# Optimization experiments

Measured on AMD Instinct MI355X. Metric: run time of the kernel, lower is better.

The kernel has to match this reference:

```python
import jax, jax.numpy as jnp
import numpy as np

N = 50000   # nodes
E = 800000  # edges (avg degree 16)
D = 128     # in/hid size
C = 64      # out classes
L = 3       # layers
EPS = 1e-5


def setup_inputs() -> dict:
    key = jax.random.key(0)
    ks = jax.random.split(key, 8)
    x = jax.random.normal(ks[0], (N, D), dtype=jnp.float32)
    src = jax.random.randint(ks[1], (E,), 0, N)
    dst = jax.random.randint(ks[2], (E,), 0, N)
    s = 1.0 / np.sqrt(D)
    Wself = jax.random.normal(ks[3], (L, D, D), dtype=jnp.float32) * s
    Wneigh = jax.random.normal(ks[4], (L, D, D), dtype=jnp.float32) * s
    b_conv = jnp.zeros((L, D), dtype=jnp.float32)
    gamma = jnp.ones((L - 1, D), dtype=jnp.float32)
    beta = jnp.zeros((L - 1, D), dtype=jnp.float32)
    Wout = jax.random.normal(ks[5], (D, C), dtype=jnp.float32) * s
    bout = jnp.zeros((C,), dtype=jnp.float32)
    return {"x": x, "src": src, "dst": dst, "Wself": Wself, "Wneigh": Wneigh,
            "b_conv": b_conv, "gamma": gamma, "beta": beta, "Wout": Wout, "bout": bout}


def _layernorm(h, g, b):
    mu = jnp.mean(h, axis=-1, keepdims=True)
    var = jnp.mean(jnp.square(h - mu), axis=-1, keepdims=True)
    return g * (h - mu) * jax.lax.rsqrt(var + EPS) + b


def reference(x, src, dst, Wself, Wneigh, b_conv, gamma, beta, Wout, bout):
    # in-degree per destination node, clamped to >= 1 (DGL mean semantics)
    deg = jax.ops.segment_sum(jnp.ones((E,), dtype=x.dtype), dst, num_segments=N)
    inv_deg = 1.0 / jnp.maximum(deg, 1.0)  # [N]
    h = x
    for i in range(L):
        h_res = h
        # mean aggregation: gather src feats, scatter-add to dst, normalize
        agg = jax.ops.segment_sum(h[src], dst, num_segments=N) * inv_deg[:, None]
        # SAGEConv: fc_self(h) + fc_neigh(agg) + bias
        h = h @ Wself[i] + agg @ Wneigh[i] + b_conv[i]
        h = h + h_res  # residual (shapes always match: D == hid)
        if i != L - 1:
            h = jax.nn.relu(h)
            h = _layernorm(h, gamma[i], beta[i])
            # dropout omitted (eval mode)
    embedding = h
    logits = embedding @ Wout + bout
    return (logits, embedding)
```

## Files before the change

kernel.cpp:

```cpp
#include <hip/hip_runtime.h>

#define NN 50000
#define EE 800000
#define DD 128
#define CC 64
#define LDA 264

#define BSH 7
#define NBKT ((NN + (1 << BSH) - 1) >> BSH)
#define BCAP 3072
#define EPB 4096

typedef unsigned short u16;
typedef unsigned int u32;
typedef __attribute__((ext_vector_type(8))) short short8;
typedef __attribute__((ext_vector_type(4))) float f32x4;

__device__ __forceinline__ float bf2f(u16 u) {
    union { u32 i; float f; } v; v.i = ((u32)u) << 16; return v.f;
}
__device__ __forceinline__ u16 f2bf(float f) {
    union { float f; u32 i; } v; v.f = f;
    u32 x = v.i;
    u32 r = x + 0x7fffu + ((x >> 16) & 1u);
    return (u16)(r >> 16);
}


__global__ __launch_bounds__(1024) void k_bucket(const int* __restrict__ src,
                                                 const int* __restrict__ dst,
                                                 int* __restrict__ bcnt,
                                                 u32* __restrict__ bkt) {
    __shared__ int cnt[NBKT];
    __shared__ int base[NBKT];
    int t = threadIdx.x;
    int e0 = blockIdx.x * EPB;
    for (int i = t; i < NBKT; i += 1024) cnt[i] = 0;
    __syncthreads();
    int bk[4], lp[4];
    u32 pk[4];
#pragma unroll
    for (int j = 0; j < 4; ++j) {
        int e = e0 + t + 1024 * j;
        if (e < EE) {
            int d = dst[e];
            int s = src[e];
            bk[j] = d >> BSH;
            pk[j] = (u32)s | ((u32)(d & 127) << 16);
            lp[j] = atomicAdd(&cnt[bk[j]], 1);
        } else {
            bk[j] = -1;
        }
    }
    __syncthreads();
    for (int i = t; i < NBKT; i += 1024)
        base[i] = atomicAdd(&bcnt[i], cnt[i]);
    __syncthreads();
#pragma unroll
    for (int j = 0; j < 4; ++j) {
        if (bk[j] >= 0)
            bkt[(size_t)bk[j] * BCAP + base[bk[j]] + lp[j]] = pk[j];
    }
}


__global__ __launch_bounds__(512) void k_fill2(const int* __restrict__ bcnt,
                                               const u32* __restrict__ bkt,
                                               int* __restrict__ row_off,
                                               float* __restrict__ inv_deg,
                                               int* __restrict__ csr) {
    __shared__ int cnt[128];
    __shared__ int off[128];
    __shared__ int wtot;
    int b = blockIdx.x;
    int t = threadIdx.x;
    int lane = t & 63;
    int n = bcnt[b];

    int part = 0;
    for (int i = lane; i < b; i += 64) part += bcnt[i];
#pragma unroll
    for (int o = 1; o < 64; o <<= 1) part += __shfl_xor(part, o);
    int gbase = part;

    if (t < 128) cnt[t] = 0;
    __syncthreads();

    const u32* bp = bkt + (size_t)b * BCAP;
    int dl[6], sv[6], lp[6];
#pragma unroll
    for (int j = 0; j < 6; ++j) {
        int i = t + 512 * j;
        if (i < n) {
            u32 pk = bp[i];
            dl[j] = (int)(pk >> 16) & 127;
            sv[j] = (int)(pk & 0xffffu);
            lp[j] = atomicAdd(&cnt[dl[j]], 1);
        } else {
            dl[j] = -1;
        }
    }
    __syncthreads();

    int x = 0, v = 0;
    if (t < 128) {
        v = cnt[t];
        x = v;
#pragma unroll
        for (int o = 1; o < 64; o <<= 1) {
            int y = __shfl_up(x, o, 64);
            if (lane >= o) x += y;
        }
        if (t == 63) wtot = x;
    }
    __syncthreads();
    if (t < 128) {
        int excl = x - v + ((t >= 64) ? wtot : 0);
        off[t] = excl;
        int node = (b << BSH) + t;
        if (node < NN) {
            row_off[node] = gbase + excl;
            inv_deg[node] = 1.0f / fmaxf((float)v, 1.0f);
        } else if (node == NN) {
            row_off[NN] = gbase + excl;
        }
    }
    __syncthreads();

    int* cp = csr + gbase;
#pragma unroll
    for (int j = 0; j < 6; ++j) {
        if (dl[j] >= 0) cp[off[dl[j]] + lp[j]] = sv[j];
    }
}


__global__ __launch_bounds__(256) void k_x2bf(const float* __restrict__ x,
                                              u16* __restrict__ xb) {
    int i = (blockIdx.x * 256 + threadIdx.x) * 4;
    if (i < NN * DD) {
        float4 v = *(const float4*)(x + i);
        uint2 p;
        p.x = (u32)f2bf(v.x) | ((u32)f2bf(v.y) << 16);
        p.y = (u32)f2bf(v.z) | ((u32)f2bf(v.w) << 16);
        *(uint2*)(xb + i) = p;
    }
}


__global__ __launch_bounds__(256) void k_wpack(const float* __restrict__ Ws,
                                               const float* __restrict__ Wn,
                                               u16* __restrict__ wpk) {
    int tid = blockIdx.x * 256 + threadIdx.x;
    if (tid >= 3 * 4096) return;
    int layer = tid >> 12;
    int rem = tid & 4095;
    int ks = rem >> 9;
    int nt = (rem >> 6) & 7;
    int lane = rem & 63;
    int n = nt * 16 + (lane & 15);
    int kb = ks * 32 + (lane >> 4) * 8;
    u16 o[8];
#pragma unroll
    for (int j = 0; j < 8; ++j) {
        int k = kb + j;
        float w = (k < DD) ? Ws[layer * DD * DD + k * DD + n]
                           : Wn[layer * DD * DD + (k - DD) * DD + n];
        o[j] = f2bf(w);
    }
    uint4 pk;
    pk.x = (u32)o[0] | ((u32)o[1] << 16);
    pk.y = (u32)o[2] | ((u32)o[3] << 16);
    pk.z = (u32)o[4] | ((u32)o[5] << 16);
    pk.w = (u32)o[6] | ((u32)o[7] << 16);
    *(uint4*)(wpk + (size_t)tid * 8) = pk;
}


__device__ __forceinline__ void acc8(float* a, uint4 u) {
    a[0] += bf2f((u16)(u.x & 0xffffu)); a[1] += bf2f((u16)(u.x >> 16));
    a[2] += bf2f((u16)(u.y & 0xffffu)); a[3] += bf2f((u16)(u.y >> 16));
    a[4] += bf2f((u16)(u.z & 0xffffu)); a[5] += bf2f((u16)(u.z >> 16));
    a[6] += bf2f((u16)(u.w & 0xffffu)); a[7] += bf2f((u16)(u.w >> 16));
}

__global__ __launch_bounds__(256) void k_layer(const float* __restrict__ h_in,
                                               const u16* __restrict__ hb,
                                               const int* __restrict__ row_off,
                                               const int* __restrict__ csr,
                                               const float* __restrict__ inv_deg,
                                               const u16* __restrict__ wpk,
                                               const float* __restrict__ bias,
                                               const float* __restrict__ gmm,
                                               const float* __restrict__ bet,
                                               float* __restrict__ h_out,
                                               u16* __restrict__ hb_out,
                                               int do_ln) {
    __shared__ u16 A[64 * LDA];
    int t = threadIdx.x;
    int b0 = blockIdx.x * 64;

#pragma unroll
    for (int j = 0; j < 4; ++j) {
        int idx = t + 256 * j;
        int r = idx >> 4;
        int c = idx & 15;
        int node = b0 + r;
        uint4 v = make_uint4(0, 0, 0, 0);
        if (node < NN) v = *(const uint4*)(hb + (size_t)node * DD + c * 8);
        *(uint4*)&A[r * LDA + c * 8] = v;
    }

    int quad = t >> 4;
    int l16 = t & 15;
#pragma unroll
    for (int nn = 0; nn < 4; ++nn) {
        int r = quad * 4 + nn;
        int node = b0 + r;
        uint4 p = make_uint4(0, 0, 0, 0);
        if (node < NN) {
            float a[8] = {0.f, 0.f, 0.f, 0.f, 0.f, 0.f, 0.f, 0.f};
            int beg = row_off[node], end = row_off[node + 1];
            int e = beg;
            for (; e + 4 <= end; e += 4) {
                int s0 = csr[e + 0], s1 = csr[e + 1];
                int s2 = csr[e + 2], s3 = csr[e + 3];
                uint4 u0 = *(const uint4*)(hb + (size_t)s0 * DD + l16 * 8);
                uint4 u1 = *(const uint4*)(hb + (size_t)s1 * DD + l16 * 8);
                uint4 u2 = *(const uint4*)(hb + (size_t)s2 * DD + l16 * 8);
                uint4 u3 = *(const uint4*)(hb + (size_t)s3 * DD + l16 * 8);
                acc8(a, u0); acc8(a, u1); acc8(a, u2); acc8(a, u3);
            }
            for (; e < end; ++e) {
                int s0 = csr[e];
                uint4 u0 = *(const uint4*)(hb + (size_t)s0 * DD + l16 * 8);
                acc8(a, u0);
            }
            float sc = inv_deg[node];
            p.x = (u32)f2bf(a[0] * sc) | ((u32)f2bf(a[1] * sc) << 16);
            p.y = (u32)f2bf(a[2] * sc) | ((u32)f2bf(a[3] * sc) << 16);
            p.z = (u32)f2bf(a[4] * sc) | ((u32)f2bf(a[5] * sc) << 16);
            p.w = (u32)f2bf(a[6] * sc) | ((u32)f2bf(a[7] * sc) << 16);
        }
        *(uint4*)&A[r * LDA + 128 + l16 * 8] = p;
    }
    __syncthreads();

    int wv = t >> 6, lane = t & 63;
    int m = lane & 15, q = lane >> 4;

    f32x4 acc[8];
#pragma unroll
    for (int nt = 0; nt < 8; ++nt) acc[nt] = (f32x4)(0.f);

    const u16* Arow = &A[(wv * 16 + m) * LDA + q * 8];
    const short8* wp = (const short8*)wpk;
#pragma unroll
    for (int ks = 0; ks < 8; ++ks) {
        short8 af = *(const short8*)(Arow + ks * 32);
        const short8* bp = wp + (ks * 8) * 64 + lane;
#pragma unroll
        for (int nt = 0; nt < 8; ++nt) {
            short8 bf = bp[nt * 64];
            acc[nt] = __builtin_amdgcn_mfma_f32_16x16x32_bf16(af, bf, acc[nt], 0, 0, 0);
        }
    }

    float bcol[8], gcol[8], ecol[8];
#pragma unroll
    for (int nt = 0; nt < 8; ++nt) {
        bcol[nt] = bias[nt * 16 + m];
        if (do_ln) { gcol[nt] = gmm[nt * 16 + m]; ecol[nt] = bet[nt * 16 + m]; }
    }

#pragma unroll
    for (int j = 0; j < 4; ++j) {
        int node = b0 + wv * 16 + q * 4 + j;
        bool ok = node < NN;
        const float* hr = h_in + (size_t)node * DD;
        float v[8];
        float s = 0.f, qq = 0.f;
#pragma unroll
        for (int nt = 0; nt < 8; ++nt) {
            float x = acc[nt][j] + bcol[nt];
            if (ok) x += hr[nt * 16 + m];
            if (do_ln) {
                x = fmaxf(x, 0.f);
                s += x; qq += x * x;
            }
            v[nt] = x;
        }
        if (do_ln) {
#pragma unroll
            for (int o = 1; o < 16; o <<= 1) {
                s += __shfl_xor(s, o);
                qq += __shfl_xor(qq, o);
            }
            float mu = s * (1.0f / 128.0f);
            float var = fmaxf(qq * (1.0f / 128.0f) - mu * mu, 0.f);
            float rs = rsqrtf(var + 1e-5f);
#pragma unroll
            for (int nt = 0; nt < 8; ++nt)
                v[nt] = gcol[nt] * (v[nt] - mu) * rs + ecol[nt];
        }
        if (ok) {
            float* orow = h_out + (size_t)node * DD;
#pragma unroll
            for (int nt = 0; nt < 8; ++nt) orow[nt * 16 + m] = v[nt];
            if (hb_out) {
                u16* brow = hb_out + (size_t)node * DD;
#pragma unroll
                for (int nt = 0; nt < 8; ++nt) brow[nt * 16 + m] = f2bf(v[nt]);
            }
        }
    }
}


__device__ __forceinline__ void stage_tile(const float* __restrict__ g, int b0,
                                           float* __restrict__ tile, int t) {
#pragma unroll
    for (int j = 0; j < 8; ++j) {
        int idx = t + 256 * j;
        int r = idx >> 5;
        int c = idx & 31;
        int node = b0 + r;
        float4 f = make_float4(0.f, 0.f, 0.f, 0.f);
        if (node < NN) f = *(const float4*)(g + (size_t)node * DD + c * 4);
        *(float4*)&tile[r * DD + c * 4] = f;
    }
}

__global__ __launch_bounds__(256) void k_logits(const float* __restrict__ h,
                                                const float* __restrict__ Wo,
                                                const float* __restrict__ bo,
                                                float* __restrict__ out) {
    __shared__ float tile[64 * DD];
    int t = threadIdx.x;
    int b0 = blockIdx.x * 64;
    int cg = t & 15;
    int ng = t >> 4;
    stage_tile(h, b0, tile, t);
    __syncthreads();
    float acc[4][4];
#pragma unroll
    for (int i = 0; i < 4; ++i)
#pragma unroll
        for (int j = 0; j < 4; ++j) acc[i][j] = 0.f;
    for (int k = 0; k < DD; k += 4) {
        float4 w0 = *(const float4*)(Wo + (k + 0) * CC + cg * 4);
        float4 w1 = *(const float4*)(Wo + (k + 1) * CC + cg * 4);
        float4 w2 = *(const float4*)(Wo + (k + 2) * CC + cg * 4);
        float4 w3 = *(const float4*)(Wo + (k + 3) * CC + cg * 4);
#pragma unroll
        for (int i = 0; i < 4; ++i) {
            float4 hv = *(const float4*)&tile[(ng * 4 + i) * DD + k];
            acc[i][0] = fmaf(hv.x, w0.x, fmaf(hv.y, w1.x, fmaf(hv.z, w2.x, fmaf(hv.w, w3.x, acc[i][0]))));
            acc[i][1] = fmaf(hv.x, w0.y, fmaf(hv.y, w1.y, fmaf(hv.z, w2.y, fmaf(hv.w, w3.y, acc[i][1]))));
            acc[i][2] = fmaf(hv.x, w0.z, fmaf(hv.y, w1.z, fmaf(hv.z, w2.z, fmaf(hv.w, w3.z, acc[i][2]))));
            acc[i][3] = fmaf(hv.x, w0.w, fmaf(hv.y, w1.w, fmaf(hv.z, w2.w, fmaf(hv.w, w3.w, acc[i][3]))));
        }
    }
    float4 b4 = *(const float4*)(bo + cg * 4);
#pragma unroll
    for (int i = 0; i < 4; ++i) {
        int node = b0 + ng * 4 + i;
        if (node < NN) {
            *(float4*)(out + (size_t)node * CC + cg * 4) =
                make_float4(acc[i][0] + b4.x, acc[i][1] + b4.y,
                            acc[i][2] + b4.z, acc[i][3] + b4.w);
        }
    }
}


extern "C" void kernel_launch(void* const* d_in, const int* in_sizes, int n_in,
                              void* d_out, int out_size, void* d_ws, size_t ws_size,
                              hipStream_t stream) {
    const float* x  = (const float*)d_in[0];
    const int* src  = (const int*)d_in[1];
    const int* dst  = (const int*)d_in[2];
    const float* Ws = (const float*)d_in[3];
    const float* Wn = (const float*)d_in[4];
    const float* bc = (const float*)d_in[5];
    const float* gm = (const float*)d_in[6];
    const float* bt = (const float*)d_in[7];
    const float* Wo = (const float*)d_in[8];
    const float* bo = (const float*)d_in[9];
    float* out = (float*)d_out;
    float* emb = out + (size_t)NN * CC;

    char* p = (char*)d_ws;
    auto alloc = [&](size_t bytes) { void* r = (void*)p; p += (bytes + 255) & ~(size_t)255; return r; };
    float* h0    = (float*)alloc((size_t)NN * DD * 4);
    float* h1    = (float*)alloc((size_t)NN * DD * 4);
    u16* xb      = (u16*)alloc((size_t)NN * DD * 2);
    u16* hb0     = (u16*)alloc((size_t)NN * DD * 2);
    u16* hb1     = (u16*)alloc((size_t)NN * DD * 2);
    u16* wpk     = (u16*)alloc((size_t)3 * 4096 * 8 * 2);
    float* invd  = (float*)alloc(NN * 4);
    int* row_off = (int*)alloc((NN + 1) * 4);
    int* bcnt    = (int*)alloc(NBKT * 4);
    int* csr     = (int*)alloc(EE * 4);
    u32* bkt     = (u32*)h1;

    hipMemsetAsync(bcnt, 0, NBKT * 4, stream);

    k_bucket<<<(EE + EPB - 1) / EPB, 1024, 0, stream>>>(src, dst, bcnt, bkt);
    k_fill2<<<NBKT, 512, 0, stream>>>(bcnt, bkt, row_off, invd, csr);
    k_x2bf<<<(NN * DD / 4 + 255) / 256, 256, 0, stream>>>(x, xb);
    k_wpack<<<(3 * 4096 + 255) / 256, 256, 0, stream>>>(Ws, Wn, wpk);

    const int NB = (NN + 63) / 64;
    k_layer<<<NB, 256, 0, stream>>>(x, xb, row_off, csr, invd,
                                    wpk + (size_t)0 * 4096 * 8,
                                    bc + 0 * DD, gm + 0 * DD, bt + 0 * DD,
                                    h0, hb0, 1);
    k_layer<<<NB, 256, 0, stream>>>(h0, hb0, row_off, csr, invd,
                                    wpk + (size_t)1 * 4096 * 8,
                                    bc + 1 * DD, gm + 1 * DD, bt + 1 * DD,
                                    h1, hb1, 1);
    k_layer<<<NB, 256, 0, stream>>>(h1, hb1, row_off, csr, invd,
                                    wpk + (size_t)2 * 4096 * 8,
                                    bc + 2 * DD, (const float*)nullptr, (const float*)nullptr,
                                    emb, (u16*)nullptr, 0);
    k_logits<<<NB, 256, 0, stream>>>(emb, Wo, bo, out);
}
```

Before: 306.9 us.

## Halve layer tile to 32 nodes and split GEMM columns across waves

Each k_layer block now processes 32 nodes instead of 64, doubling the grid. The four waves are arranged 2x2 over rows and output columns, so each wave computes 16 rows by 64 columns. LayerNorm row statistics are combined across the two column-half waves through shared memory and an extra barrier. The aim is more blocks and smaller LDS per block for better occupancy and latency hiding in the gather-bound aggregation, at the cost of reloading weights per block and an added sync.

```diff
diff --git a/kernel.cpp b/kernel.cpp
--- a/kernel.cpp
+++ b/kernel.cpp
@@ -196,12 +196,14 @@
                                                float* __restrict__ h_out,
                                                u16* __restrict__ hb_out,
                                                int do_ln) {
-    __shared__ u16 A[64 * LDA];
+    __shared__ u16 A[32 * LDA];
+    __shared__ float lnS[2][32];
+    __shared__ float lnQ[2][32];
     int t = threadIdx.x;
-    int b0 = blockIdx.x * 64;
-
-#pragma unroll
-    for (int j = 0; j < 4; ++j) {
+    int b0 = blockIdx.x * 32;
+
+#pragma unroll
+    for (int j = 0; j < 2; ++j) {
         int idx = t + 256 * j;
         int r = idx >> 4;
         int c = idx & 15;
@@ -214,8 +216,8 @@
     int quad = t >> 4;
     int l16 = t & 15;
 #pragma unroll
-    for (int nn = 0; nn < 4; ++nn) {
-        int r = quad * 4 + nn;
+    for (int nn = 0; nn < 2; ++nn) {
+        int r = quad * 2 + nn;
         int node = b0 + r;
         uint4 p = make_uint4(0, 0, 0, 0);
         if (node < NN) {
@@ -247,48 +249,51 @@
     __syncthreads();
 
     int wv = t >> 6, lane = t & 63;
+    int wr = wv >> 1, wc = wv & 1;
     int m = lane & 15, q = lane >> 4;
 
-    f32x4 acc[8];
-#pragma unroll
-    for (int nt = 0; nt < 8; ++nt) acc[nt] = (f32x4)(0.f);
-
-    const u16* Arow = &A[(wv * 16 + m) * LDA + q * 8];
+    f32x4 acc[4];
+#pragma unroll
+    for (int nt = 0; nt < 4; ++nt) acc[nt] = (f32x4)(0.f);
+
+    const u16* Arow = &A[(wr * 16 + m) * LDA + q * 8];
     const short8* wp = (const short8*)wpk;
 #pragma unroll
     for (int ks = 0; ks < 8; ++ks) {
         short8 af = *(const short8*)(Arow + ks * 32);
-        const short8* bp = wp + (ks * 8) * 64 + lane;
-#pragma unroll
-        for (int nt = 0; nt < 8; ++nt) {
+        const short8* bp = wp + (ks * 8 + wc * 4) * 64 + lane;
+#pragma unroll
+        for (int nt = 0; nt < 4; ++nt) {
             short8 bf = bp[nt * 64];
             acc[nt] = __builtin_amdgcn_mfma_f32_16x16x32_bf16(af, bf, acc[nt], 0, 0, 0);
         }
     }
 
-    float bcol[8], gcol[8], ecol[8];
-#pragma unroll
-    for (int nt = 0; nt < 8; ++nt) {
-        bcol[nt] = bias[nt * 16 + m];
-        if (do_ln) { gcol[nt] = gmm[nt * 16 + m]; ecol[nt] = bet[nt * 16 + m]; }
-    }
-
+    float bcol[4], gcol[4], ecol[4];
+#pragma unroll
+    for (int nt = 0; nt < 4; ++nt) {
+        int col = wc * 64 + nt * 16 + m;
+        bcol[nt] = bias[col];
+        if (do_ln) { gcol[nt] = gmm[col]; ecol[nt] = bet[col]; }
+    }
+
+    float v[4][4];
 #pragma unroll
     for (int j = 0; j < 4; ++j) {
-        int node = b0 + wv * 16 + q * 4 + j;
+        int row = wr * 16 + q * 4 + j;
+        int node = b0 + row;
         bool ok = node < NN;
         const float* hr = h_in + (size_t)node * DD;
-        float v[8];
         float s = 0.f, qq = 0.f;
 #pragma unroll
-        for (int nt = 0; nt < 8; ++nt) {
+        for (int nt = 0; nt < 4; ++nt) {
             float x = acc[nt][j] + bcol[nt];
-            if (ok) x += hr[nt * 16 + m];
+            if (ok) x += hr[wc * 64 + nt * 16 + m];
             if (do_ln) {
                 x = fmaxf(x, 0.f);
                 s += x; qq += x * x;
             }
-            v[nt] = x;
+            v[j][nt] = x;
         }
         if (do_ln) {
 #pragma unroll
@@ -296,21 +301,34 @@
                 s += __shfl_xor(s, o);
                 qq += __shfl_xor(qq, o);
             }
+            if (m == 0) { lnS[wc][row] = s; lnQ[wc][row] = qq; }
+        }
+    }
+    if (do_ln) __syncthreads();
+
+#pragma unroll
+    for (int j = 0; j < 4; ++j) {
+        int row = wr * 16 + q * 4 + j;
+        int node = b0 + row;
+        bool ok = node < NN;
+        if (do_ln) {
+            float s = lnS[0][row] + lnS[1][row];
+            float qq = lnQ[0][row] + lnQ[1][row];
             float mu = s * (1.0f / 128.0f);
             float var = fmaxf(qq * (1.0f / 128.0f) - mu * mu, 0.f);
             float rs = rsqrtf(var + 1e-5f);
 #pragma unroll
-            for (int nt = 0; nt < 8; ++nt)
-                v[nt] = gcol[nt] * (v[nt] - mu) * rs + ecol[nt];
+            for (int nt = 0; nt < 4; ++nt)
+                v[j][nt] = gcol[nt] * (v[j][nt] - mu) * rs + ecol[nt];
         }
         if (ok) {
             float* orow = h_out + (size_t)node * DD;
 #pragma unroll
-            for (int nt = 0; nt < 8; ++nt) orow[nt * 16 + m] = v[nt];
+            for (int nt = 0; nt < 4; ++nt) orow[wc * 64 + nt * 16 + m] = v[j][nt];
             if (hb_out) {
                 u16* brow = hb_out + (size_t)node * DD;
 #pragma unroll
-                for (int nt = 0; nt < 8; ++nt) brow[nt * 16 + m] = f2bf(v[nt]);
+                for (int nt = 0; nt < 4; ++nt) brow[wc * 64 + nt * 16 + m] = f2bf(v[j][nt]);
             }
         }
     }
@@ -411,18 +429,18 @@
     k_x2bf<<<(NN * DD / 4 + 255) / 256, 256, 0, stream>>>(x, xb);
     k_wpack<<<(3 * 4096 + 255) / 256, 256, 0, stream>>>(Ws, Wn, wpk);
 
-    const int NB = (NN + 63) / 64;
-    k_layer<<<NB, 256, 0, stream>>>(x, xb, row_off, csr, invd,
-                                    wpk + (size_t)0 * 4096 * 8,
-                                    bc + 0 * DD, gm + 0 * DD, bt + 0 * DD,
-                                    h0, hb0, 1);
-    k_layer<<<NB, 256, 0, stream>>>(h0, hb0, row_off, csr, invd,
-                                    wpk + (size_t)1 * 4096 * 8,
-                                    bc + 1 * DD, gm + 1 * DD, bt + 1 * DD,
-                                    h1, hb1, 1);
-    k_layer<<<NB, 256, 0, stream>>>(h1, hb1, row_off, csr, invd,
-                                    wpk + (size_t)2 * 4096 * 8,
-                                    bc + 2 * DD, (const float*)nullptr, (const float*)nullptr,
-                                    emb, (u16*)nullptr, 0);
-    k_logits<<<NB, 256, 0, stream>>>(emb, Wo, bo, out);
-}
+    const int NB32 = (NN + 31) / 32;
+    k_layer<<<NB32, 256, 0, stream>>>(x, xb, row_off, csr, invd,
+                                      wpk + (size_t)0 * 4096 * 8,
+                                      bc + 0 * DD, gm + 0 * DD, bt + 0 * DD,
+                                      h0, hb0, 1);
+    k_layer<<<NB32, 256, 0, stream>>>(h0, hb0, row_off, csr, invd,
+                                      wpk + (size_t)1 * 4096 * 8,
+                                      bc + 1 * DD, gm + 1 * DD, bt + 1 * DD,
+                                      h1, hb1, 1);
+    k_layer<<<NB32, 256, 0, stream>>>(h1, hb1, row_off, csr, invd,
+                                      wpk + (size_t)2 * 4096 * 8,
+                                      bc + 2 * DD, (const float*)nullptr, (const float*)nullptr,
+                                      emb, (u16*)nullptr, 0);
+    k_logits<<<(NN + 63) / 64, 256, 0, stream>>>(emb, Wo, bo, out);
+}
```

Measured after the change: 308.8 us. Within noise of the previous version (+0.6%).

## Fuse output logits projection into final layer kernel using bf16 MFMA

Applied to the files above, without the earlier changes.

Removes the separate fp32 logits kernel. The last SAGE layer now writes its embedding tile to shared memory as bf16 and computes logits with MFMA on prepacked Wout fragments. This avoids re-reading the embedding from global memory and saves one launch. It adds an extra bf16 rounding of the embedding before the output projection and needs more registers in the final layer.

```diff
diff --git a/kernel.cpp b/kernel.cpp
--- a/kernel.cpp
+++ b/kernel.cpp
@@ -10,6 +10,9 @@
 #define NBKT ((NN + (1 << BSH) - 1) >> BSH)
 #define BCAP 3072
 #define EPB 4096
+
+#define NFRAG_L 4096
+#define NFRAG_O 1024
 
 typedef unsigned short u16;
 typedef unsigned int u32;
@@ -150,23 +153,35 @@
 
 __global__ __launch_bounds__(256) void k_wpack(const float* __restrict__ Ws,
                                                const float* __restrict__ Wn,
+                                               const float* __restrict__ Wo,
                                                u16* __restrict__ wpk) {
     int tid = blockIdx.x * 256 + threadIdx.x;
-    if (tid >= 3 * 4096) return;
-    int layer = tid >> 12;
-    int rem = tid & 4095;
-    int ks = rem >> 9;
-    int nt = (rem >> 6) & 7;
-    int lane = rem & 63;
-    int n = nt * 16 + (lane & 15);
-    int kb = ks * 32 + (lane >> 4) * 8;
+    if (tid >= 3 * NFRAG_L + NFRAG_O) return;
+    int lane = tid & 63;
     u16 o[8];
-#pragma unroll
-    for (int j = 0; j < 8; ++j) {
-        int k = kb + j;
-        float w = (k < DD) ? Ws[layer * DD * DD + k * DD + n]
-                           : Wn[layer * DD * DD + (k - DD) * DD + n];
-        o[j] = f2bf(w);
+    if (tid < 3 * NFRAG_L) {
+        int layer = tid >> 12;
+        int rem = tid & 4095;
+        int ks = rem >> 9;
+        int nt = (rem >> 6) & 7;
+        int n = nt * 16 + (lane & 15);
+        int kb = ks * 32 + (lane >> 4) * 8;
+#pragma unroll
+        for (int j = 0; j < 8; ++j) {
+            int k = kb + j;
+            float w = (k < DD) ? Ws[layer * DD * DD + k * DD + n]
+                               : Wn[layer * DD * DD + (k - DD) * DD + n];
+            o[j] = f2bf(w);
+        }
+    } else {
+        int rem = tid - 3 * NFRAG_L;
+        int ks = rem >> 8;
+        int nt = (rem >> 6) & 3;
+        int n = nt * 16 + (lane & 15);
+        int kb = ks * 32 + (lane >> 4) * 8;
+#pragma unroll
+        for (int j = 0; j < 8; ++j)
+            o[j] = f2bf(Wo[(kb + j) * CC + n]);
     }
     uint4 pk;
     pk.x = (u32)o[0] | ((u32)o[1] << 16);
@@ -195,7 +210,10 @@
                                                const float* __restrict__ bet,
                                                float* __restrict__ h_out,
                                                u16* __restrict__ hb_out,
-                                               int do_ln) {
+                                               int do_ln,
+                                               const u16* __restrict__ wpo,
+                                               const float* __restrict__ bo,
+                                               float* __restrict__ lg) {
     __shared__ u16 A[64 * LDA];
     int t = threadIdx.x;
     int b0 = blockIdx.x * 64;
@@ -273,6 +291,8 @@
         if (do_ln) { gcol[nt] = gmm[nt * 16 + m]; ecol[nt] = bet[nt * 16 + m]; }
     }
 
+    float v2[4][8];
+
 #pragma unroll
     for (int j = 0; j < 4; ++j) {
         int node = b0 + wv * 16 + q * 4 + j;
@@ -313,62 +333,48 @@
                 for (int nt = 0; nt < 8; ++nt) brow[nt * 16 + m] = f2bf(v[nt]);
             }
         }
-    }
-}
-
-
-__device__ __forceinline__ void stage_tile(const float* __restrict__ g, int b0,
-                                           float* __restrict__ tile, int t) {
-#pragma unroll
-    for (int j = 0; j < 8; ++j) {
-        int idx = t + 256 * j;
-        int r = idx >> 5;
-        int c = idx & 31;
-        int node = b0 + r;
-        float4 f = make_float4(0.f, 0.f, 0.f, 0.f);
-        if (node < NN) f = *(const float4*)(g + (size_t)node * DD + c * 4);
-        *(float4*)&tile[r * DD + c * 4] = f;
-    }
-}
-
-__global__ __launch_bounds__(256) void k_logits(const float* __restrict__ h,
-                                                const float* __restrict__ Wo,
-                                                const float* __restrict__ bo,
-                                                float* __restrict__ out) {
-    __shared__ float tile[64 * DD];
-    int t = threadIdx.x;
-    int b0 = blockIdx.x * 64;
-    int cg = t & 15;
-    int ng = t >> 4;
-    stage_tile(h, b0, tile, t);
-    __syncthreads();
-    float acc[4][4];
-#pragma unroll
-    for (int i = 0; i < 4; ++i)
-#pragma unroll
-        for (int j = 0; j < 4; ++j) acc[i][j] = 0.f;
-    for (int k = 0; k < DD; k += 4) {
-        float4 w0 = *(const float4*)(Wo + (k + 0) * CC + cg * 4);
-        float4 w1 = *(const float4*)(Wo + (k + 1) * CC + cg * 4);
-        float4 w2 = *(const float4*)(Wo + (k + 2) * CC + cg * 4);
-        float4 w3 = *(const float4*)(Wo + (k + 3) * CC + cg * 4);
-#pragma unroll
-        for (int i = 0; i < 4; ++i) {
-            float4 hv = *(const float4*)&tile[(ng * 4 + i) * DD + k];
-            acc[i][0] = fmaf(hv.x, w0.x, fmaf(hv.y, w1.x, fmaf(hv.z, w2.x, fmaf(hv.w, w3.x, acc[i][0]))));
-            acc[i][1] = fmaf(hv.x, w0.y, fmaf(hv.y, w1.y, fmaf(hv.z, w2.y, fmaf(hv.w, w3.y, acc[i][1]))));
-            acc[i][2] = fmaf(hv.x, w0.z, fmaf(hv.y, w1.z, fmaf(hv.z, w2.z, fmaf(hv.w, w3.z, acc[i][2]))));
-            acc[i][3] = fmaf(hv.x, w0.w, fmaf(hv.y, w1.w, fmaf(hv.z, w2.w, fmaf(hv.w, w3.w, acc[i][3]))));
-        }
-    }
-    float4 b4 = *(const float4*)(bo + cg * 4);
-#pragma unroll
-    for (int i = 0; i < 4; ++i) {
-        int node = b0 + ng * 4 + i;
-        if (node < NN) {
-            *(float4*)(out + (size_t)node * CC + cg * 4) =
-                make_float4(acc[i][0] + b4.x, acc[i][1] + b4.y,
-                            acc[i][2] + b4.z, acc[i][3] + b4.w);
+        if (lg) {
+#pragma unroll
+            for (int nt = 0; nt < 8; ++nt) v2[j][nt] = v[nt];
+        }
+    }
+
+    if (lg) {
+        __syncthreads();
+#pragma unroll
+        for (int j = 0; j < 4; ++j) {
+            int row = wv * 16 + q * 4 + j;
+            int node = b0 + row;
+            if (node < NN) {
+#pragma unroll
+                for (int nt = 0; nt < 8; ++nt)
+                    A[row * LDA + nt * 16 + m] = f2bf(v2[j][nt]);
+            }
+        }
+        __syncthreads();
+        f32x4 fa[4];
+#pragma unroll
+        for (int nt = 0; nt < 4; ++nt) fa[nt] = (f32x4)(0.f);
+        const u16* Ar2 = &A[(wv * 16 + m) * LDA + q * 8];
+        const short8* bpo = (const short8*)wpo;
+#pragma unroll
+        for (int ks = 0; ks < 4; ++ks) {
+            short8 af = *(const short8*)(Ar2 + ks * 32);
+            const short8* bp = bpo + (ks * 4) * 64 + lane;
+#pragma unroll
+            for (int nt = 0; nt < 4; ++nt) {
+                short8 bf = bp[nt * 64];
+                fa[nt] = __builtin_amdgcn_mfma_f32_16x16x32_bf16(af, bf, fa[nt], 0, 0, 0);
+            }
+        }
+#pragma unroll
+        for (int j = 0; j < 4; ++j) {
+            int node = b0 + wv * 16 + q * 4 + j;
+            if (node < NN) {
+#pragma unroll
+                for (int nt = 0; nt < 4; ++nt)
+                    lg[(size_t)node * CC + nt * 16 + m] = fa[nt][j] + bo[nt * 16 + m];
+            }
         }
     }
 }
@@ -397,7 +403,7 @@
     u16* xb      = (u16*)alloc((size_t)NN * DD * 2);
     u16* hb0     = (u16*)alloc((size_t)NN * DD * 2);
     u16* hb1     = (u16*)alloc((size_t)NN * DD * 2);
-    u16* wpk     = (u16*)alloc((size_t)3 * 4096 * 8 * 2);
+    u16* wpk     = (u16*)alloc((size_t)(3 * NFRAG_L + NFRAG_O) * 8 * 2);
     float* invd  = (float*)alloc(NN * 4);
     int* row_off = (int*)alloc((NN + 1) * 4);
     int* bcnt    = (int*)alloc(NBKT * 4);
@@ -409,20 +415,22 @@
     k_bucket<<<(EE + EPB - 1) / EPB, 1024, 0, stream>>>(src, dst, bcnt, bkt);
     k_fill2<<<NBKT, 512, 0, stream>>>(bcnt, bkt, row_off, invd, csr);
     k_x2bf<<<(NN * DD / 4 + 255) / 256, 256, 0, stream>>>(x, xb);
-    k_wpack<<<(3 * 4096 + 255) / 256, 256, 0, stream>>>(Ws, Wn, wpk);
+    k_wpack<<<(3 * NFRAG_L + NFRAG_O + 255) / 256, 256, 0, stream>>>(Ws, Wn, Wo, wpk);
 
     const int NB = (NN + 63) / 64;
     k_layer<<<NB, 256, 0, stream>>>(x, xb, row_off, csr, invd,
-                                    wpk + (size_t)0 * 4096 * 8,
+                                    wpk + (size_t)0 * NFRAG_L * 8,
                                     bc + 0 * DD, gm + 0 * DD, bt + 0 * DD,
-                                    h0, hb0, 1);
+                                    h0, hb0, 1,
+                                    (const u16*)nullptr, (const float*)nullptr, (float*)nullptr);
     k_layer<<<NB, 256, 0, stream>>>(h0, hb0, row_off, csr, invd,
-                                    wpk + (size_t)1 * 4096 * 8,
+                                    wpk + (size_t)1 * NFRAG_L * 8,
                                     bc + 1 * DD, gm + 1 * DD, bt + 1 * DD,
-                                    h1, hb1, 1);
+                                    h1, hb1, 1,
+                                    (const u16*)nullptr, (const float*)nullptr, (float*)nullptr);
     k_layer<<<NB, 256, 0, stream>>>(h1, hb1, row_off, csr, invd,
-                                    wpk + (size_t)2 * 4096 * 8,
+                                    wpk + (size_t)2 * NFRAG_L * 8,
                                     bc + 2 * DD, (const float*)nullptr, (const float*)nullptr,
-                                    emb, (u16*)nullptr, 0);
-    k_logits<<<NB, 256, 0, stream>>>(emb, Wo, bo, out);
-}
+                                    emb, (u16*)nullptr, 0,
+                                    wpk + (size_t)3 * NFRAG_L * 8, bo, out);
+}
```

After: 372.9 us. 21.5% more time.
